# Kernel optimization log

Measured on AMD Instinct MI355X. Metric: run time of the kernel, lower is better.

## Reference

```python
import jax, jax.numpy as jnp
import numpy as np

B, A, FEAT = 16, 256, 64
HID = 256
TEMB = 32
NUM_T = 100
L = 4
E = 131072
N = B * A


def _remove_mean(x):
    # x: [B, A, 3]
    return x - jnp.mean(x, axis=1, keepdims=True)


def setup_inputs() -> dict:
    key = jax.random.key(0)
    ks = jax.random.split(key, 24)
    s = 0.02
    inp = {
        "h": jax.random.normal(ks[0], (B, A, FEAT), jnp.float32),
        "x0": jax.random.normal(ks[1], (B, A, 3), jnp.float32),
        "noise": jax.random.normal(ks[2], (B, A, 3), jnp.float32),
        "t": jax.random.randint(ks[3], (B,), 0, NUM_T, jnp.int32),
        "row": jax.random.randint(ks[4], (E,), 0, N, jnp.int32),
        "col": jax.random.randint(ks[5], (E,), 0, N, jnp.int32),
        # node embedding
        "W_emb": jax.random.normal(ks[6], (FEAT + TEMB, HID), jnp.float32) * s,
        "b_emb": jnp.zeros((HID,), jnp.float32),
        # per-layer EGNN params, stacked over L layers
        "eW1": jax.random.normal(ks[7], (L, 2 * HID + 1, HID), jnp.float32) * s,
        "eb1": jnp.zeros((L, HID), jnp.float32),
        "eW2": jax.random.normal(ks[8], (L, HID, HID), jnp.float32) * s,
        "eb2": jnp.zeros((L, HID), jnp.float32),
        "cW1": jax.random.normal(ks[9], (L, HID, HID), jnp.float32) * s,
        "cb1": jnp.zeros((L, HID), jnp.float32),
        "cW2": jax.random.normal(ks[10], (L, HID, 1), jnp.float32) * s,
        "nW1": jax.random.normal(ks[11], (L, 2 * HID, HID), jnp.float32) * s,
        "nb1": jnp.zeros((L, HID), jnp.float32),
        "nW2": jax.random.normal(ks[12], (L, HID, HID), jnp.float32) * s,
        "nb2": jnp.zeros((L, HID), jnp.float32),
    }
    return inp


def _time_embedding(t):
    half = TEMB // 2
    freq = jnp.exp(jnp.arange(half, dtype=jnp.float32) * (-np.log(10000.0) / (half - 1)))
    ang = t.astype(jnp.float32)[:, None] * freq[None, :]  # [B, half]
    return jnp.concatenate([jnp.sin(ang), jnp.cos(ang)], axis=-1)  # [B, TEMB]


def _egnn_layer(h, x, row, col, eW1, eb1, eW2, eb2, cW1, cb1, cW2, nW1, nb1, nW2, nb2):
    coord_diff = x[row] - x[col]                                  # [E, 3]
    radial = jnp.sum(coord_diff * coord_diff, axis=1, keepdims=True)  # [E, 1]
    edge_in = jnp.concatenate([h[row], h[col], radial], axis=1)   # [E, 2H+1]
    m = jax.nn.silu(edge_in @ eW1 + eb1)
    m_ij = jax.nn.silu(m @ eW2 + eb2)                             # [E, H]
    w = jax.nn.silu(m_ij @ cW1 + cb1) @ cW2                       # [E, 1]
    coord_update = coord_diff * w                                 # [E, 3]
    x_new = x + jax.ops.segment_sum(coord_update, row, num_segments=N)
    m_i = jax.ops.segment_sum(m_ij, row, num_segments=N)          # [N, H]
    node_in = jnp.concatenate([h, m_i], axis=1)
    h_new = h + (jax.nn.silu(node_in @ nW1 + nb1) @ nW2 + nb2)
    return h_new, x_new


def reference(h, x0, noise, W_emb, b_emb, eW1, eb1, eW2, eb2, cW1, cb1, cW2,
              nW1, nb1, nW2, nb2, t, row, col):
    # diffusion schedule
    betas = jnp.linspace(1e-4, 0.02, NUM_T, dtype=jnp.float32)
    alphas_cumprod = jnp.cumprod(1.0 - betas)
    # forward diffusion q(x_t | x_0)
    noise = _remove_mean(noise)
    ab = alphas_cumprod[t][:, None, None]                          # [B,1,1]
    xt = jnp.sqrt(ab) * x0 + jnp.sqrt(1.0 - ab) * noise
    xt = _remove_mean(xt)

    t_emb = _time_embedding(t)                                     # [B, TEMB]
    t_emb_flat = jnp.repeat(t_emb, A, axis=0)                      # [N, TEMB]
    h_flat = h.reshape(N, FEAT)
    xt_flat = xt.reshape(N, 3)
    h_in = jnp.concatenate([h_flat, t_emb_flat], axis=-1)

    hh = h_in @ W_emb + b_emb                                      # [N, H]
    xx = xt_flat
    for l in range(L):
        hh, xx = _egnn_layer(hh, xx, row, col,
                             eW1[l], eb1[l], eW2[l], eb2[l],
                             cW1[l], cb1[l], cW2[l],
                             nW1[l], nb1[l], nW2[l], nb2[l])

    noise_pred = (xx - xt_flat).reshape(B, A, 3)
    noise_pred = _remove_mean(noise_pred)
    loss = jnp.mean((noise_pred - noise) ** 2)
    return loss
```

## Files before the change

### kernel.cpp

```cpp
#include <hip/hip_runtime.h>

#define NB 16
#define NA 256
#define NNODES 4096
#define FEATD 64
#define HID 256
#define TEMBD 32
#define NUMT 100
#define NE 131072
#define NL 4
#define NCHUNK (NE / 16)

typedef __attribute__((ext_vector_type(8))) short short8;
typedef __attribute__((ext_vector_type(4))) float f32x4;
typedef __attribute__((ext_vector_type(2))) float f32x2;

__device__ __forceinline__ float silu_f(float v) {
    float s = __builtin_amdgcn_rcpf(1.f + __builtin_amdgcn_exp2f(-1.44269504f * v));
    return v * s;
}

__device__ __forceinline__ short f2bf(float f) {
    union { float f; unsigned u; } v; v.f = f;
    unsigned r = (v.u + 0x7fffu + ((v.u >> 16) & 1u)) >> 16;
    return (short)r;
}
__device__ __forceinline__ short f2bf_t(float f) {
    union { float f; unsigned u; } v; v.f = f;
    return (short)(v.u >> 16);
}
__device__ __forceinline__ float bf2f(short s) {
    union { float f; unsigned u; } v; v.u = ((unsigned)(unsigned short)s) << 16;
    return v.f;
}

__device__ __forceinline__ float block_sum(float v, float* red, int a) {
    red[a] = v; __syncthreads();
    for (int s = 128; s > 0; s >>= 1) {
        if (a < s) red[a] += red[a + s];
        __syncthreads();
    }
    float r = red[0]; __syncthreads();
    return r;
}

__global__ __launch_bounds__(256) void prep_kernel(
    const float* __restrict__ x0, const float* __restrict__ noise,
    const int* __restrict__ t,
    float* __restrict__ noise_c, float* __restrict__ xt, float* __restrict__ temb)
{
    __shared__ float red[256];
    __shared__ float sab_s[2];
    int b = blockIdx.x, a = threadIdx.x;
    int base = (b * NA + a) * 3;

    float nx = noise[base + 0], ny = noise[base + 1], nz = noise[base + 2];
    float mnx = block_sum(nx, red, a) * (1.f / NA);
    float mny = block_sum(ny, red, a) * (1.f / NA);
    float mnz = block_sum(nz, red, a) * (1.f / NA);
    nx -= mnx; ny -= mny; nz -= mnz;
    noise_c[base + 0] = nx; noise_c[base + 1] = ny; noise_c[base + 2] = nz;

    if (a == 0) {
        int tt = t[b];
        float p = 1.f;
        for (int i = 0; i < NUMT; i++) {
            float beta = 1e-4f + (0.02f - 1e-4f) * (float)i / (float)(NUMT - 1);
            if (i <= tt) p *= (1.f - beta);
        }
        sab_s[0] = sqrtf(p);
        sab_s[1] = sqrtf(1.f - p);
    }
    __syncthreads();
    float sab = sab_s[0], s1ab = sab_s[1];

    float xx = sab * x0[base + 0] + s1ab * nx;
    float xy = sab * x0[base + 1] + s1ab * ny;
    float xz = sab * x0[base + 2] + s1ab * nz;
    float mx = block_sum(xx, red, a) * (1.f / NA);
    float my = block_sum(xy, red, a) * (1.f / NA);
    float mz = block_sum(xz, red, a) * (1.f / NA);
    xt[base + 0] = xx - mx; xt[base + 1] = xy - my; xt[base + 2] = xz - mz;

    if (a < TEMBD / 2) {
        float fr = expf(-logf(10000.f) * (float)a / (float)(TEMBD / 2 - 1));
        float ang = (float)t[b] * fr;
        temb[b * TEMBD + a] = sinf(ang);
        temb[b * TEMBD + TEMBD / 2 + a] = cosf(ang);
    }
}

__global__ __launch_bounds__(256) void csr_hist(const int* __restrict__ row, int* __restrict__ deg)
{
    int i = blockIdx.x * 256 + threadIdx.x;
    if (i < NE) atomicAdd(&deg[row[i]], 1);
}

__global__ __launch_bounds__(256) void csr_scan(const int* __restrict__ deg, int* __restrict__ cursor)
{
    __shared__ int s[256];
    int t = threadIdx.x;
    int base = t * 16;
    int loc[16];
    int sum = 0;
    for (int i = 0; i < 16; i++) { loc[i] = sum; sum += deg[base + i]; }
    s[t] = sum; __syncthreads();
    for (int off = 1; off < 256; off <<= 1) {
        int v = (t >= off) ? s[t - off] : 0;
        __syncthreads();
        s[t] += v;
        __syncthreads();
    }
    int excl = (t == 0) ? 0 : s[t - 1];
    for (int i = 0; i < 16; i++) cursor[base + i] = excl + loc[i];
}

__global__ __launch_bounds__(256) void csr_scatter(
    const int* __restrict__ row, const int* __restrict__ col,
    int* __restrict__ cursor, int* __restrict__ prow, int* __restrict__ pcol)
{
    int i = blockIdx.x * 256 + threadIdx.x;
    if (i < NE) {
        int r = row[i];
        int p = atomicAdd(&cursor[r], 1);
        prow[p] = r;
        pcol[p] = col[i];
    }
}

#define WOFF_EMB 0
#define WOFF_L(l) (24576 + (l) * 458752)
#define WOFF_AB 0
#define WOFF_E2 131072
#define WOFF_C1 196608
#define WOFF_N1 262144
#define WOFF_N2 393216
#define W_TOTAL (24576 + 4 * 458752)

__global__ __launch_bounds__(256) void convert_weights(
    const float* __restrict__ W_emb, const float* __restrict__ eW1,
    const float* __restrict__ eW2, const float* __restrict__ cW1,
    const float* __restrict__ nW1, const float* __restrict__ nW2,
    short* __restrict__ wb)
{
    int idx = blockIdx.x * 256 + threadIdx.x;
    if (idx >= W_TOTAL) return;
    if (idx < 24576) {
        int k = idx >> 8, n = idx & 255;
        wb[WOFF_EMB + ((k >> 5) << 13) + (n << 5) + (k & 31)] = f2bf(W_emb[idx]);
        return;
    }
    int r = idx - 24576;
    int l = r / 458752;
    int o = r - l * 458752;
    if (o < 131072) {
        int k = o >> 9, n = o & 511;
        const float* src = eW1 + (size_t)l * 513 * 256 +
            (n < 256 ? (size_t)k * 256 + n : (size_t)(256 + k) * 256 + (n - 256));
        wb[WOFF_L(l) + WOFF_AB + ((k >> 5) * 16384) + (n << 5) + (k & 31)] = f2bf(*src);
        return;
    }
    const float* src; int dst; int o2;
    if (o < 196608)      { o2 = o - 131072; src = eW2 + (size_t)l * 65536 + o2;  dst = WOFF_L(l) + WOFF_E2; }
    else if (o < 262144) { o2 = o - 196608; src = cW1 + (size_t)l * 65536 + o2;  dst = WOFF_L(l) + WOFF_C1; }
    else if (o < 393216) { o2 = o - 262144; src = nW1 + (size_t)l * 131072 + o2; dst = WOFF_L(l) + WOFF_N1; }
    else                 { o2 = o - 393216; src = nW2 + (size_t)l * 65536 + o2;  dst = WOFF_L(l) + WOFF_N2; }
    int k = o2 >> 8, n = o2 & 255;
    wb[dst + ((k >> 5) << 13) + (n << 5) + (k & 31)] = f2bf(*src);
}

#define WF8_TOTAL (4 * 2 * 65536)
__global__ __launch_bounds__(256) void convert_weights_fp8(
    const float* __restrict__ eW2, const float* __restrict__ cW1,
    char* __restrict__ wf8)
{
    int idx = blockIdx.x * 256 + threadIdx.x;
    if (idx >= WF8_TOTAL) return;
    int l = idx >> 17;
    int o = idx & 131071;
    int mat = o >> 16;
    int o2 = o & 65535;
    int k = o2 >> 8, n = o2 & 255;
    const float* src = (mat == 0 ? eW2 : cW1) + (size_t)l * 65536 + (size_t)k * 256 + n;
    float v = (*src) * 16.f;
    int p = __builtin_amdgcn_cvt_pk_fp8_f32(v, v, 0, false);
    wf8[(size_t)l * 131072 + mat * 65536 + (k >> 5) * 8192 + n * 32 + (k & 31)] = (char)(p & 0xff);
}

__global__ __launch_bounds__(256) void build_hin(
    const float* __restrict__ h, const float* __restrict__ temb, short* __restrict__ hin)
{
    int idx = blockIdx.x * 256 + threadIdx.x;
    int n = idx / 96;
    int k = idx - n * 96;
    float v = (k < FEATD) ? h[n * FEATD + k] : temb[(n >> 8) * TEMBD + (k - FEATD)];
    hin[idx] = f2bf(v);
}

__global__ __launch_bounds__(512) void emb_p12_fused(
    const short* __restrict__ hin, const short* __restrict__ wtEmb,
    const float* __restrict__ b_emb, const short* __restrict__ wtAB,
    const float* __restrict__ eb1_0,
    short* __restrict__ hh, short* __restrict__ P12)
{
    __shared__ short h2s[16 * 264];
    int tid = threadIdx.x;
    int wv = tid >> 6, l = tid & 63;
    int lr = l & 15, q = l >> 4;
    int r0 = blockIdx.x * 16;

    f32x4 acc[2];
    #pragma unroll
    for (int i = 0; i < 2; i++) acc[i] = (f32x4){0.f, 0.f, 0.f, 0.f};
    #pragma unroll
    for (int kt = 0; kt < 3; kt++) {
        int kk = kt * 32 + q * 8;
        short8 fa = *(const short8*)&hin[(size_t)(r0 + lr) * 96 + kk];
        #pragma unroll
        for (int nt = 0; nt < 2; nt++) {
            short8 fb = *(const short8*)&wtEmb[kt * 8192 + (wv * 32 + nt * 16 + lr) * 32 + q * 8];
            acc[nt] = __builtin_amdgcn_mfma_f32_16x16x32_bf16(fa, fb, acc[nt], 0, 0, 0);
        }
    }
    #pragma unroll
    for (int nt = 0; nt < 2; nt++) {
        int col = wv * 32 + nt * 16 + lr;
        float bv = b_emb[col];
        #pragma unroll
        for (int rg = 0; rg < 4; rg++) {
            int rrow = q * 4 + rg;
            short b = f2bf(acc[nt][rg] + bv);
            hh[(size_t)(r0 + rrow) * 256 + col] = b;
            h2s[rrow * 264 + col] = b;
        }
    }
    __syncthreads();

    f32x4 acc3[4];
    #pragma unroll
    for (int i = 0; i < 4; i++) acc3[i] = (f32x4){0.f, 0.f, 0.f, 0.f};
    #pragma unroll 2
    for (int kt = 0; kt < 8; kt++) {
        short8 fa = *(const short8*)&h2s[lr * 264 + kt * 32 + q * 8];
        #pragma unroll
        for (int nt = 0; nt < 4; nt++) {
            short8 fb = *(const short8*)&wtAB[kt * 16384 + (wv * 64 + nt * 16 + lr) * 32 + q * 8];
            acc3[nt] = __builtin_amdgcn_mfma_f32_16x16x32_bf16(fa, fb, acc3[nt], 0, 0, 0);
        }
    }
    #pragma unroll
    for (int nt = 0; nt < 4; nt++) {
        int col = wv * 64 + nt * 16 + lr;
        float bv = (col < 256) ? eb1_0[col] : 0.f;
        #pragma unroll
        for (int rg = 0; rg < 4; rg++)
            P12[(size_t)(r0 + q * 4 + rg) * 512 + col] = f2bf(acc3[nt][rg] + bv);
    }
}

__global__ __launch_bounds__(512) void node_p12_fused(
    const short* __restrict__ hc, const float* __restrict__ m_i,
    const int* __restrict__ cursor,
    const int* __restrict__ tag0, const int* __restrict__ tag1,
    const float* __restrict__ msl0, const float* __restrict__ msl1,
    const float* __restrict__ xsl0, const float* __restrict__ xsl1,
    const float* __restrict__ x_agg, float* __restrict__ x_cur,
    const short* __restrict__ wtN1, const float* __restrict__ nb1,
    const short* __restrict__ wtN2, const float* __restrict__ nb2,
    const short* __restrict__ wtAB, const float* __restrict__ eb1n,
    short* __restrict__ hn, short* __restrict__ P12)
{
    __shared__ short m_is[16 * 264];
    __shared__ short t1s[16 * 264];
    __shared__ short h2s[16 * 264];
    int tid = threadIdx.x;
    int wv = tid >> 6, l = tid & 63;
    int lr = l & 15, q = l >> 4;
    int r0 = blockIdx.x * 16;

    {
        int rr = tid >> 5;
        int cc = (tid & 31) * 8;
        int r = r0 + rr;
        float v[8];
        const float* mrow = &m_i[(size_t)r * 256 + cc];
        #pragma unroll
        for (int i = 0; i < 8; i++) v[i] = mrow[i];
        int end = cursor[r];
        int start = (r == 0) ? 0 : cursor[r - 1];
        if (end > start) {
            int cs = start >> 4, ce = (end - 1) >> 4;
            for (int ch = cs; ch <= ce; ch++) {
                if (tag0[ch] == r) {
                    const float* s0 = &msl0[(size_t)ch * 256 + cc];
                    #pragma unroll
                    for (int i = 0; i < 8; i++) v[i] += s0[i];
                }
                if (tag1[ch] == r) {
                    const float* s1 = &msl1[(size_t)ch * 256 + cc];
                    #pragma unroll
                    for (int i = 0; i < 8; i++) v[i] += s1[i];
                }
            }
        }
        #pragma unroll
        for (int i = 0; i < 8; i++) m_is[rr * 264 + cc + i] = f2bf(v[i]);
        if (tid < 16) {
            int r2 = r0 + tid;
            float sx = x_agg[r2 * 3 + 0], sy = x_agg[r2 * 3 + 1], sz = x_agg[r2 * 3 + 2];
            int end2 = cursor[r2];
            int start2 = (r2 == 0) ? 0 : cursor[r2 - 1];
            if (end2 > start2) {
                int cs2 = start2 >> 4, ce2 = (end2 - 1) >> 4;
                for (int ch = cs2; ch <= ce2; ch++) {
                    if (tag0[ch] == r2) { sx += xsl0[ch * 3 + 0]; sy += xsl0[ch * 3 + 1]; sz += xsl0[ch * 3 + 2]; }
                    if (tag1[ch] == r2) { sx += xsl1[ch * 3 + 0]; sy += xsl1[ch * 3 + 1]; sz += xsl1[ch * 3 + 2]; }
                }
            }
            x_cur[r2 * 3 + 0] += sx;
            x_cur[r2 * 3 + 1] += sy;
            x_cur[r2 * 3 + 2] += sz;
        }
    }
    __syncthreads();

    f32x4 acc[2];
    #pragma unroll
    for (int i = 0; i < 2; i++) acc[i] = (f32x4){0.f, 0.f, 0.f, 0.f};
    #pragma unroll 2
    for (int kt = 0; kt < 16; kt++) {
        int kk = kt * 32 + q * 8;
        short8 fa;
        if (kk < 256) fa = *(const short8*)&hc[(size_t)(r0 + lr) * 256 + kk];
        else          fa = *(const short8*)&m_is[lr * 264 + kk - 256];
        #pragma unroll
        for (int nt = 0; nt < 2; nt++) {
            short8 fb = *(const short8*)&wtN1[kt * 8192 + (wv * 32 + nt * 16 + lr) * 32 + q * 8];
            acc[nt] = __builtin_amdgcn_mfma_f32_16x16x32_bf16(fa, fb, acc[nt], 0, 0, 0);
        }
    }
    #pragma unroll
    for (int nt = 0; nt < 2; nt++) {
        int col = wv * 32 + nt * 16 + lr;
        float bv = nb1[col];
        #pragma unroll
        for (int rg = 0; rg < 4; rg++)
            t1s[(q * 4 + rg) * 264 + col] = f2bf_t(silu_f(acc[nt][rg] + bv));
    }
    __syncthreads();

    f32x4 acc2[2];
    #pragma unroll
    for (int i = 0; i < 2; i++) acc2[i] = (f32x4){0.f, 0.f, 0.f, 0.f};
    #pragma unroll 2
    for (int kt = 0; kt < 8; kt++) {
        short8 fa = *(const short8*)&t1s[lr * 264 + kt * 32 + q * 8];
        #pragma unroll
        for (int nt = 0; nt < 2; nt++) {
            short8 fb = *(const short8*)&wtN2[kt * 8192 + (wv * 32 + nt * 16 + lr) * 32 + q * 8];
            acc2[nt] = __builtin_amdgcn_mfma_f32_16x16x32_bf16(fa, fb, acc2[nt], 0, 0, 0);
        }
    }
    #pragma unroll
    for (int nt = 0; nt < 2; nt++) {
        int col = wv * 32 + nt * 16 + lr;
        float bv = nb2[col];
        #pragma unroll
        for (int rg = 0; rg < 4; rg++) {
            int rrow = q * 4 + rg;
            float v = acc2[nt][rg] + bv + bf2f(hc[(size_t)(r0 + rrow) * 256 + col]);
            short b = f2bf(v);
            hn[(size_t)(r0 + rrow) * 256 + col] = b;
            h2s[rrow * 264 + col] = b;
        }
    }
    __syncthreads();

    f32x4 acc3[4];
    #pragma unroll
    for (int i = 0; i < 4; i++) acc3[i] = (f32x4){0.f, 0.f, 0.f, 0.f};
    #pragma unroll 2
    for (int kt = 0; kt < 8; kt++) {
        short8 fa = *(const short8*)&h2s[lr * 264 + kt * 32 + q * 8];
        #pragma unroll
        for (int nt = 0; nt < 4; nt++) {
            short8 fb = *(const short8*)&wtAB[kt * 16384 + (wv * 64 + nt * 16 + lr) * 32 + q * 8];
            acc3[nt] = __builtin_amdgcn_mfma_f32_16x16x32_bf16(fa, fb, acc3[nt], 0, 0, 0);
        }
    }
    #pragma unroll
    for (int nt = 0; nt < 4; nt++) {
        int col = wv * 64 + nt * 16 + lr;
        float bv = (col < 256) ? eb1n[col] : 0.f;
        #pragma unroll
        for (int rg = 0; rg < 4; rg++)
            P12[(size_t)(r0 + q * 4 + rg) * 512 + col] = f2bf(acc3[nt][rg] + bv);
    }
}

__global__ __launch_bounds__(256, 4) void egnn_edge_mfma(
    const short* __restrict__ P12, const float* __restrict__ x,
    const int* __restrict__ prow, const int* __restrict__ pcol,
    const float* __restrict__ w512,
    const char* __restrict__ wf8E2, const float* __restrict__ eb2,
    const char* __restrict__ wf8C1, const float* __restrict__ cb1,
    const float* __restrict__ cW2,
    float* __restrict__ m_i, float* __restrict__ x_agg,
    float* __restrict__ msl0, float* __restrict__ msl1,
    float* __restrict__ xsl0, float* __restrict__ xsl1,
    int* __restrict__ tag0, int* __restrict__ tag1, int do_mi)
{
    __shared__ __align__(16) char m_lds[64 * 272];
    __shared__ float cd_s[64][3];
    __shared__ int prow_s[64];
    __shared__ float wred[4][64];
    __shared__ float xtmp[64][3];

    int tid = threadIdx.x;
    int e0 = blockIdx.x * 64;
    int wv = tid >> 6, l = tid & 63;
    int lr = l & 15, q = l >> 4;

    {
        int e = tid >> 2, cq = tid & 3;
        int r = prow[e0 + e], c = pcol[e0 + e];
        float dx = x[r * 3 + 0] - x[c * 3 + 0];
        float dy = x[r * 3 + 1] - x[c * 3 + 1];
        float dz = x[r * 3 + 2] - x[c * 3 + 2];
        float rad = dx * dx + dy * dy + dz * dz;
        if (cq == 0) {
            prow_s[e] = r;
            cd_s[e][0] = dx; cd_s[e][1] = dy; cd_s[e][2] = dz;
        }
        const short* p1r = P12 + (size_t)r * 512;
        const short* p2r = P12 + (size_t)c * 512 + 256;
        #pragma unroll
        for (int j = 0; j < 8; j++) {
            int cb = (j >> 1) * 64 + (j & 1) * 32 + cq * 8;
            short8 a = *(const short8*)&p1r[cb];
            short8 b = *(const short8*)&p2r[cb];
            float4 w0 = *(const float4*)&w512[cb];
            float4 w1 = *(const float4*)&w512[cb + 4];
            float wv8[8] = {w0.x, w0.y, w0.z, w0.w, w1.x, w1.y, w1.z, w1.w};
            float s[8];
            #pragma unroll
            for (int k2 = 0; k2 < 8; k2++)
                s[k2] = silu_f(bf2f(a[k2]) + bf2f(b[k2]) + rad * wv8[k2]);
            int lo = __builtin_amdgcn_cvt_pk_fp8_f32(s[0], s[1], 0, false);
            lo = __builtin_amdgcn_cvt_pk_fp8_f32(s[2], s[3], lo, true);
            int hi = __builtin_amdgcn_cvt_pk_fp8_f32(s[4], s[5], 0, false);
            hi = __builtin_amdgcn_cvt_pk_fp8_f32(s[6], s[7], hi, true);
            int2 d = {lo, hi};
            *(int2*)&m_lds[e * 272 + cb] = d;
        }
    }
    __syncthreads();

    f32x4 acc[4][4];
    #pragma unroll
    for (int i = 0; i < 4; i++)
        #pragma unroll
        for (int j = 0; j < 4; j++) acc[i][j] = (f32x4){0.f, 0.f, 0.f, 0.f};
    #pragma unroll 2
    for (int kt = 0; kt < 8; kt++) {
        long fa[4], fb[4];
        #pragma unroll
        for (int mt = 0; mt < 4; mt++)
            fa[mt] = *(const long*)&m_lds[(mt * 16 + lr) * 272 + kt * 32 + q * 8];
        #pragma unroll
        for (int nt = 0; nt < 4; nt++)
            fb[nt] = *(const long*)&wf8E2[kt * 8192 + (wv * 64 + nt * 16 + lr) * 32 + q * 8];
        #pragma unroll
        for (int mt = 0; mt < 4; mt++)
            #pragma unroll
            for (int nt = 0; nt < 4; nt++)
                acc[mt][nt] = __builtin_amdgcn_mfma_f32_16x16x32_fp8_fp8(fa[mt], fb[nt], acc[mt][nt], 0, 0, 0);
    }
    __syncthreads();
    #pragma unroll
    for (int nt = 0; nt < 4; nt++) {
        int ccol = wv * 64 + nt * 16 + lr;
        float b2 = eb2[ccol];
        #pragma unroll
        for (int mt = 0; mt < 4; mt++)
            #pragma unroll
            for (int rg = 0; rg < 4; rg++) {
                int e = mt * 16 + q * 4 + rg;
                float v = silu_f(fmaf(acc[mt][nt][rg], 0.0625f, b2));
                int p = __builtin_amdgcn_cvt_pk_fp8_f32(v, v, 0, false);
                m_lds[e * 272 + ccol] = (char)(p & 0xff);
            }
    }
    __syncthreads();

    #pragma unroll
    for (int i = 0; i < 4; i++)
        #pragma unroll
        for (int j = 0; j < 4; j++) acc[i][j] = (f32x4){0.f, 0.f, 0.f, 0.f};
    #pragma unroll 2
    for (int kt = 0; kt < 8; kt++) {
        long fa[4], fb[4];
        #pragma unroll
        for (int mt = 0; mt < 4; mt++)
            fa[mt] = *(const long*)&m_lds[(mt * 16 + lr) * 272 + kt * 32 + q * 8];
        #pragma unroll
        for (int nt = 0; nt < 4; nt++)
            fb[nt] = *(const long*)&wf8C1[kt * 8192 + (wv * 64 + nt * 16 + lr) * 32 + q * 8];
        #pragma unroll
        for (int mt = 0; mt < 4; mt++)
            #pragma unroll
            for (int nt = 0; nt < 4; nt++)
                acc[mt][nt] = __builtin_amdgcn_mfma_f32_16x16x32_fp8_fp8(fa[mt], fb[nt], acc[mt][nt], 0, 0, 0);
    }

    if (do_mi) {
        int ebase = wv * 16;
        int c4 = l * 4;
        int chunk = blockIdx.x * 4 + wv;
        float a0 = 0.f, a1 = 0.f, a2 = 0.f, a3 = 0.f;
        int cur = prow_s[ebase];
        int nrun = 0;
        #pragma unroll
        for (int j = 0; j < 16; j++) {
            int e = ebase + j;
            int r = prow_s[e];
            if (r != cur) {
                float4 v = {a0, a1, a2, a3};
                if (nrun == 0) *(float4*)&msl0[(size_t)chunk * 256 + c4] = v;
                else           *(float4*)&m_i[(size_t)cur * 256 + c4] = v;
                nrun++; a0 = a1 = a2 = a3 = 0.f; cur = r;
            }
            int mv = *(const int*)&m_lds[e * 272 + c4];
            f32x2 lo = __builtin_amdgcn_cvt_pk_f32_fp8(mv, false);
            f32x2 hi = __builtin_amdgcn_cvt_pk_f32_fp8(mv, true);
            a0 += lo.x; a1 += lo.y; a2 += hi.x; a3 += hi.y;
        }
        float4 v = {a0, a1, a2, a3};
        if (nrun == 0) *(float4*)&msl0[(size_t)chunk * 256 + c4] = v;
        else           *(float4*)&msl1[(size_t)chunk * 256 + c4] = v;
        if (l == 0) {
            tag0[chunk] = prow_s[ebase];
            tag1[chunk] = nrun ? cur : -1;
        }
    }

    {
        float wp[4][4];
        #pragma unroll
        for (int i = 0; i < 4; i++)
            #pragma unroll
            for (int j = 0; j < 4; j++) wp[i][j] = 0.f;
        #pragma unroll
        for (int nt = 0; nt < 4; nt++) {
            int ccol = wv * 64 + nt * 16 + lr;
            float b1 = cb1[ccol];
            float c2 = cW2[ccol];
            #pragma unroll
            for (int mt = 0; mt < 4; mt++)
                #pragma unroll
                for (int rg = 0; rg < 4; rg++)
                    wp[mt][rg] += silu_f(fmaf(acc[mt][nt][rg], 0.0625f, b1)) * c2;
        }
        #pragma unroll
        for (int mt = 0; mt < 4; mt++)
            #pragma unroll
            for (int rg = 0; rg < 4; rg++) {
                float v = wp[mt][rg];
                v += __shfl_xor(v, 1, 64);
                v += __shfl_xor(v, 2, 64);
                v += __shfl_xor(v, 4, 64);
                v += __shfl_xor(v, 8, 64);
                if (lr == 0) wred[wv][mt * 16 + q * 4 + rg] = v;
            }
    }
    __syncthreads();
    if (tid < 64) {
        float w = wred[0][tid] + wred[1][tid] + wred[2][tid] + wred[3][tid];
        xtmp[tid][0] = cd_s[tid][0] * w;
        xtmp[tid][1] = cd_s[tid][1] * w;
        xtmp[tid][2] = cd_s[tid][2] * w;
    }
    __syncthreads();
    if (tid < 64) {
        int e = tid, j = e & 15, cw = e >> 4;
        int r = prow_s[e];
        bool leader = (j == 0) || (prow_s[e - 1] != r);
        if (leader) {
            int eend = (cw + 1) * 16;
            float sx = 0.f, sy = 0.f, sz = 0.f;
            int k = e;
            while (k < eend && prow_s[k] == r) {
                sx += xtmp[k][0]; sy += xtmp[k][1]; sz += xtmp[k][2]; k++;
            }
            int chunk = blockIdx.x * 4 + cw;
            if (j == 0)        { xsl0[chunk * 3 + 0] = sx; xsl0[chunk * 3 + 1] = sy; xsl0[chunk * 3 + 2] = sz; }
            else if (k == eend){ xsl1[chunk * 3 + 0] = sx; xsl1[chunk * 3 + 1] = sy; xsl1[chunk * 3 + 2] = sz; }
            else               { x_agg[r * 3 + 0] = sx; x_agg[r * 3 + 1] = sy; x_agg[r * 3 + 2] = sz; }
        }
    }
}

__global__ __launch_bounds__(256) void loss_part(
    const float* __restrict__ x_cur, const float* __restrict__ xt,
    const float* __restrict__ nc,
    const int* __restrict__ cursor,
    const int* __restrict__ tag0, const int* __restrict__ tag1,
    const float* __restrict__ xsl0, const float* __restrict__ xsl1,
    const float* __restrict__ x_agg,
    float* __restrict__ lpart)
{
    __shared__ float red[256];
    int b = blockIdx.x, a = threadIdx.x;
    int n = b * NA + a;
    int base = n * 3;

    float sx = x_agg[base + 0], sy = x_agg[base + 1], sz = x_agg[base + 2];
    int end = cursor[n];
    int start = (n == 0) ? 0 : cursor[n - 1];
    if (end > start) {
        int cs = start >> 4, ce = (end - 1) >> 4;
        for (int ch = cs; ch <= ce; ch++) {
            if (tag0[ch] == n) { sx += xsl0[ch * 3 + 0]; sy += xsl0[ch * 3 + 1]; sz += xsl0[ch * 3 + 2]; }
            if (tag1[ch] == n) { sx += xsl1[ch * 3 + 0]; sy += xsl1[ch * 3 + 1]; sz += xsl1[ch * 3 + 2]; }
        }
    }
    float px = x_cur[base + 0] + sx - xt[base + 0];
    float py = x_cur[base + 1] + sy - xt[base + 1];
    float pz = x_cur[base + 2] + sz - xt[base + 2];
    float mx = block_sum(px, red, a) * (1.f / NA);
    float my = block_sum(py, red, a) * (1.f / NA);
    float mz = block_sum(pz, red, a) * (1.f / NA);
    px -= mx; py -= my; pz -= mz;
    float dx = px - nc[base + 0], dy = py - nc[base + 1], dz = pz - nc[base + 2];
    float s = block_sum(dx * dx + dy * dy + dz * dz, red, a);
    if (a == 0) lpart[b] = s;
}

__global__ void loss_final(const float* __restrict__ lpart, float* __restrict__ out)
{
    if (threadIdx.x == 0) {
        float s = 0.f;
        for (int i = 0; i < NB; i++) s += lpart[i];
        out[0] = s / (float)(NNODES * 3);
    }
}

extern "C" void kernel_launch(void* const* d_in, const int* in_sizes, int n_in,
                              void* d_out, int out_size, void* d_ws, size_t ws_size,
                              hipStream_t stream)
{
    (void)in_sizes; (void)n_in; (void)out_size; (void)ws_size;
    const float* h     = (const float*)d_in[0];
    const float* x0    = (const float*)d_in[1];
    const float* noise = (const float*)d_in[2];
    const int*   t     = (const int*)d_in[3];
    const int*   row   = (const int*)d_in[4];
    const int*   col   = (const int*)d_in[5];
    const float* W_emb = (const float*)d_in[6];
    const float* b_emb = (const float*)d_in[7];
    const float* eW1   = (const float*)d_in[8];
    const float* eb1   = (const float*)d_in[9];
    const float* eW2   = (const float*)d_in[10];
    const float* eb2   = (const float*)d_in[11];
    const float* cW1   = (const float*)d_in[12];
    const float* cb1   = (const float*)d_in[13];
    const float* cW2   = (const float*)d_in[14];
    const float* nW1   = (const float*)d_in[15];
    const float* nb1   = (const float*)d_in[16];
    const float* nW2   = (const float*)d_in[17];
    const float* nb2   = (const float*)d_in[18];

    float* f = (float*)d_ws;
    size_t fo = 0;
    float* temb    = f + fo; fo += NB * TEMBD;
    float* noise_c = f + fo; fo += NNODES * 3;
    float* xt      = f + fo; fo += NNODES * 3;
    float* x_cur   = f + fo; fo += NNODES * 3;
    float* x_agg   = f + fo; fo += NNODES * 3;
    float* m_i     = f + fo; fo += (size_t)NNODES * HID;
    float* lpart   = f + fo; fo += NB;
    float* msl0    = f + fo; fo += (size_t)NCHUNK * 256;
    float* msl1    = f + fo; fo += (size_t)NCHUNK * 256;
    float* xsl0    = f + fo; fo += (size_t)NCHUNK * 3;
    float* xsl1    = f + fo; fo += (size_t)NCHUNK * 3;

    int* iw = (int*)(f + fo);
    size_t io = 0;
    int* deg    = iw + io; io += NNODES;
    int* cursor = iw + io; io += NNODES;
    int* prow   = iw + io; io += NE;
    int* pcol   = iw + io; io += NE;
    int* tag0   = iw + io; io += NCHUNK;
    int* tag1   = iw + io; io += NCHUNK;

    size_t sbase_bytes = ((((char*)(iw + io)) - (char*)d_ws) + 15) & ~(size_t)15;
    short* sb = (short*)((char*)d_ws + sbase_bytes);
    short* wb  = sb;
    size_t so = W_TOTAL;
    short* hin = sb + so; so += (size_t)NNODES * 96;
    short* hh  = sb + so; so += (size_t)NNODES * HID;
    short* hh2 = sb + so; so += (size_t)NNODES * HID;
    short* P12 = sb + so; so += (size_t)NNODES * 512;
    char* wf8 = (char*)(sb + so);

    prep_kernel<<<NB, 256, 0, stream>>>(x0, noise, t, noise_c, xt, temb);
    hipMemsetAsync(deg, 0, NNODES * sizeof(int), stream);
    csr_hist<<<NE / 256, 256, 0, stream>>>(row, deg);
    csr_scan<<<1, 256, 0, stream>>>(deg, cursor);
    csr_scatter<<<NE / 256, 256, 0, stream>>>(row, col, cursor, prow, pcol);
    convert_weights<<<(W_TOTAL + 255) / 256, 256, 0, stream>>>(W_emb, eW1, eW2, cW1, nW1, nW2, wb);
    convert_weights_fp8<<<WF8_TOTAL / 256, 256, 0, stream>>>(eW2, cW1, wf8);
    build_hin<<<(NNODES * 96) / 256, 256, 0, stream>>>(h, temb, hin);
    emb_p12_fused<<<NNODES / 16, 512, 0, stream>>>(
        hin, wb + WOFF_EMB, b_emb, wb + WOFF_L(0) + WOFF_AB, eb1, hh, P12);
    hipMemcpyAsync(x_cur, xt, (size_t)NNODES * 3 * sizeof(float), hipMemcpyDeviceToDevice, stream);

    short* hc = hh;
    short* hn = hh2;
    for (int l = 0; l < NL; l++) {
        const short* wl = wb + WOFF_L(l);
        const char* wf8l = wf8 + (size_t)l * 131072;
        int last = (l == NL - 1);
        size_t zcount = last ? (size_t)(NNODES * 3)
                             : (size_t)(NNODES * 3 + NNODES * HID);
        hipMemsetAsync(x_agg, 0, zcount * sizeof(float), stream);
        egnn_edge_mfma<<<NE / 64, 256, 0, stream>>>(
            P12, x_cur, prow, pcol,
            eW1 + (size_t)l * 513 * 256 + 512 * 256,
            wf8l, eb2 + (size_t)l * HID,
            wf8l + 65536, cb1 + (size_t)l * HID,
            cW2 + (size_t)l * HID,
            m_i, x_agg, msl0, msl1, xsl0, xsl1, tag0, tag1, last ? 0 : 1);
        if (!last) {
            node_p12_fused<<<NNODES / 16, 512, 0, stream>>>(
                hc, m_i, cursor, tag0, tag1, msl0, msl1,
                xsl0, xsl1, x_agg, x_cur,
                wl + WOFF_N1, nb1 + (size_t)l * HID,
                wl + WOFF_N2, nb2 + (size_t)l * HID,
                wb + WOFF_L(l + 1) + WOFF_AB, eb1 + (size_t)(l + 1) * HID,
                hn, P12);
            short* tmp = hc; hc = hn; hn = tmp;
        }
    }

    loss_part<<<NB, 256, 0, stream>>>(
        x_cur, xt, noise_c, cursor, tag0, tag1, xsl0, xsl1, x_agg, lpart);
    loss_final<<<1, 64, 0, stream>>>(lpart, (float*)d_out);
}
```

Before: 452.2 us.

## Drop per-layer memsets via interior-node flags, fuse build_hin and loss_final

Adds a csr_flag kernel that marks nodes whose edge ranges sit strictly inside a 16-edge chunk, so only those nodes read the atomically accumulated m_i/x_agg buffers. This lets the per-layer memsets of x_agg and m_i be removed. The deg memset moves into prep_kernel, build_hin is folded into emb_p12_fused with on-the-fly bf16 conversion, and loss_final is replaced by an atomicAdd into the output. The node and embedding kernels move to 1024-thread blocks with one 16-column tile per wave. Correctness depends on the edge kernel writing every non-flagged node's contribution only through the chunk slots, and on the atomic sum's ordering.

Result: faster. 440.5 us (-2.6%).

```diff
diff --git a/kernel.cpp b/kernel.cpp
--- a/kernel.cpp
+++ b/kernel.cpp
@@ -47,12 +47,16 @@
 __global__ __launch_bounds__(256) void prep_kernel(
     const float* __restrict__ x0, const float* __restrict__ noise,
     const int* __restrict__ t,
-    float* __restrict__ noise_c, float* __restrict__ xt, float* __restrict__ temb)
+    float* __restrict__ noise_c, float* __restrict__ xt, float* __restrict__ temb,
+    int* __restrict__ deg, float* __restrict__ out)
 {
     __shared__ float red[256];
     __shared__ float sab_s[2];
     int b = blockIdx.x, a = threadIdx.x;
     int base = (b * NA + a) * 3;
+
+    deg[b * 256 + a] = 0;
+    if (b == 0 && a == 0) out[0] = 0.f;
 
     float nx = noise[base + 0], ny = noise[base + 1], nz = noise[base + 2];
     float mnx = block_sum(nx, red, a) * (1.f / NA);
@@ -128,6 +132,25 @@
     }
 }
 
+__global__ __launch_bounds__(256) void csr_flag(
+    const int* __restrict__ cursor, int* __restrict__ flag)
+{
+    int r = blockIdx.x * 256 + threadIdx.x;
+    if (r >= NNODES) return;
+    int end = cursor[r];
+    int start = (r == 0) ? 0 : cursor[r - 1];
+    int fl = 0;
+    if (end > start) {
+        int cs = start >> 4, ce = (end - 1) >> 4;
+        for (int ch = cs; ch <= ce; ch++) {
+            int rs = start > ch * 16 ? start : ch * 16;
+            int re = end < ch * 16 + 16 ? end : ch * 16 + 16;
+            if (rs > ch * 16 && re < ch * 16 + 16) fl = 1;
+        }
+    }
+    flag[r] = fl;
+}
+
 #define WOFF_EMB 0
 #define WOFF_L(l) (24576 + (l) * 458752)
 #define WOFF_AB 0
@@ -187,18 +210,9 @@
     wf8[(size_t)l * 131072 + mat * 65536 + (k >> 5) * 8192 + n * 32 + (k & 31)] = (char)(p & 0xff);
 }
 
-__global__ __launch_bounds__(256) void build_hin(
-    const float* __restrict__ h, const float* __restrict__ temb, short* __restrict__ hin)
-{
-    int idx = blockIdx.x * 256 + threadIdx.x;
-    int n = idx / 96;
-    int k = idx - n * 96;
-    float v = (k < FEATD) ? h[n * FEATD + k] : temb[(n >> 8) * TEMBD + (k - FEATD)];
-    hin[idx] = f2bf(v);
-}
-
-__global__ __launch_bounds__(512) void emb_p12_fused(
-    const short* __restrict__ hin, const short* __restrict__ wtEmb,
+__global__ __launch_bounds__(1024) void emb_p12_fused(
+    const float* __restrict__ h, const float* __restrict__ temb,
+    const short* __restrict__ wtEmb,
     const float* __restrict__ b_emb, const short* __restrict__ wtAB,
     const float* __restrict__ eb1_0,
     short* __restrict__ hh, short* __restrict__ P12)
@@ -209,48 +223,47 @@
     int lr = l & 15, q = l >> 4;
     int r0 = blockIdx.x * 16;
 
-    f32x4 acc[2];
-    #pragma unroll
-    for (int i = 0; i < 2; i++) acc[i] = (f32x4){0.f, 0.f, 0.f, 0.f};
+    f32x4 acc = (f32x4){0.f, 0.f, 0.f, 0.f};
+    int col0 = wv * 16 + lr;
+    int n = r0 + lr;
     #pragma unroll
     for (int kt = 0; kt < 3; kt++) {
         int kk = kt * 32 + q * 8;
-        short8 fa = *(const short8*)&hin[(size_t)(r0 + lr) * 96 + kk];
+        const float* src = (kk < 64) ? &h[(size_t)n * 64 + kk]
+                                     : &temb[(n >> 8) * 32 + kk - 64];
+        short8 fa;
+        #pragma unroll
+        for (int k2 = 0; k2 < 8; k2++) fa[k2] = f2bf(src[k2]);
+        short8 fb = *(const short8*)&wtEmb[kt * 8192 + col0 * 32 + q * 8];
+        acc = __builtin_amdgcn_mfma_f32_16x16x32_bf16(fa, fb, acc, 0, 0, 0);
+    }
+    {
+        float bv = b_emb[col0];
+        #pragma unroll
+        for (int rg = 0; rg < 4; rg++) {
+            int rrow = q * 4 + rg;
+            short b = f2bf(acc[rg] + bv);
+            hh[(size_t)(r0 + rrow) * 256 + col0] = b;
+            h2s[rrow * 264 + col0] = b;
+        }
+    }
+    __syncthreads();
+
+    f32x4 acc3[2];
+    #pragma unroll
+    for (int i = 0; i < 2; i++) acc3[i] = (f32x4){0.f, 0.f, 0.f, 0.f};
+    #pragma unroll 2
+    for (int kt = 0; kt < 8; kt++) {
+        short8 fa = *(const short8*)&h2s[lr * 264 + kt * 32 + q * 8];
         #pragma unroll
         for (int nt = 0; nt < 2; nt++) {
-            short8 fb = *(const short8*)&wtEmb[kt * 8192 + (wv * 32 + nt * 16 + lr) * 32 + q * 8];
-            acc[nt] = __builtin_amdgcn_mfma_f32_16x16x32_bf16(fa, fb, acc[nt], 0, 0, 0);
+            short8 fb = *(const short8*)&wtAB[kt * 16384 + (wv * 32 + nt * 16 + lr) * 32 + q * 8];
+            acc3[nt] = __builtin_amdgcn_mfma_f32_16x16x32_bf16(fa, fb, acc3[nt], 0, 0, 0);
         }
     }
     #pragma unroll
     for (int nt = 0; nt < 2; nt++) {
         int col = wv * 32 + nt * 16 + lr;
-        float bv = b_emb[col];
-        #pragma unroll
-        for (int rg = 0; rg < 4; rg++) {
-            int rrow = q * 4 + rg;
-            short b = f2bf(acc[nt][rg] + bv);
-            hh[(size_t)(r0 + rrow) * 256 + col] = b;
-            h2s[rrow * 264 + col] = b;
-        }
-    }
-    __syncthreads();
-
-    f32x4 acc3[4];
-    #pragma unroll
-    for (int i = 0; i < 4; i++) acc3[i] = (f32x4){0.f, 0.f, 0.f, 0.f};
-    #pragma unroll 2
-    for (int kt = 0; kt < 8; kt++) {
-        short8 fa = *(const short8*)&h2s[lr * 264 + kt * 32 + q * 8];
-        #pragma unroll
-        for (int nt = 0; nt < 4; nt++) {
-            short8 fb = *(const short8*)&wtAB[kt * 16384 + (wv * 64 + nt * 16 + lr) * 32 + q * 8];
-            acc3[nt] = __builtin_amdgcn_mfma_f32_16x16x32_bf16(fa, fb, acc3[nt], 0, 0, 0);
-        }
-    }
-    #pragma unroll
-    for (int nt = 0; nt < 4; nt++) {
-        int col = wv * 64 + nt * 16 + lr;
         float bv = (col < 256) ? eb1_0[col] : 0.f;
         #pragma unroll
         for (int rg = 0; rg < 4; rg++)
@@ -258,9 +271,9 @@
     }
 }
 
-__global__ __launch_bounds__(512) void node_p12_fused(
+__global__ __launch_bounds__(1024) void node_p12_fused(
     const short* __restrict__ hc, const float* __restrict__ m_i,
-    const int* __restrict__ cursor,
+    const int* __restrict__ cursor, const int* __restrict__ flag,
     const int* __restrict__ tag0, const int* __restrict__ tag1,
     const float* __restrict__ msl0, const float* __restrict__ msl1,
     const float* __restrict__ xsl0, const float* __restrict__ xsl1,
@@ -279,35 +292,37 @@
     int r0 = blockIdx.x * 16;
 
     {
-        int rr = tid >> 5;
-        int cc = (tid & 31) * 8;
+        int rr = tid >> 6;
+        int cc = (tid & 63) * 4;
         int r = r0 + rr;
-        float v[8];
-        const float* mrow = &m_i[(size_t)r * 256 + cc];
-        #pragma unroll
-        for (int i = 0; i < 8; i++) v[i] = mrow[i];
+        float v[4] = {0.f, 0.f, 0.f, 0.f};
+        if (flag[r]) {
+            float4 mv = *(const float4*)&m_i[(size_t)r * 256 + cc];
+            v[0] = mv.x; v[1] = mv.y; v[2] = mv.z; v[3] = mv.w;
+        }
         int end = cursor[r];
         int start = (r == 0) ? 0 : cursor[r - 1];
         if (end > start) {
             int cs = start >> 4, ce = (end - 1) >> 4;
             for (int ch = cs; ch <= ce; ch++) {
                 if (tag0[ch] == r) {
-                    const float* s0 = &msl0[(size_t)ch * 256 + cc];
-                    #pragma unroll
-                    for (int i = 0; i < 8; i++) v[i] += s0[i];
+                    float4 s0 = *(const float4*)&msl0[(size_t)ch * 256 + cc];
+                    v[0] += s0.x; v[1] += s0.y; v[2] += s0.z; v[3] += s0.w;
                 }
                 if (tag1[ch] == r) {
-                    const float* s1 = &msl1[(size_t)ch * 256 + cc];
-                    #pragma unroll
-                    for (int i = 0; i < 8; i++) v[i] += s1[i];
+                    float4 s1 = *(const float4*)&msl1[(size_t)ch * 256 + cc];
+                    v[0] += s1.x; v[1] += s1.y; v[2] += s1.z; v[3] += s1.w;
                 }
             }
         }
         #pragma unroll
-        for (int i = 0; i < 8; i++) m_is[rr * 264 + cc + i] = f2bf(v[i]);
+        for (int i = 0; i < 4; i++) m_is[rr * 264 + cc + i] = f2bf(v[i]);
         if (tid < 16) {
             int r2 = r0 + tid;
-            float sx = x_agg[r2 * 3 + 0], sy = x_agg[r2 * 3 + 1], sz = x_agg[r2 * 3 + 2];
+            float sx = 0.f, sy = 0.f, sz = 0.f;
+            if (flag[r2]) {
+                sx = x_agg[r2 * 3 + 0]; sy = x_agg[r2 * 3 + 1]; sz = x_agg[r2 * 3 + 2];
+            }
             int end2 = cursor[r2];
             int start2 = (r2 == 0) ? 0 : cursor[r2 - 1];
             if (end2 > start2) {
@@ -324,73 +339,60 @@
     }
     __syncthreads();
 
-    f32x4 acc[2];
-    #pragma unroll
-    for (int i = 0; i < 2; i++) acc[i] = (f32x4){0.f, 0.f, 0.f, 0.f};
+    int col0 = wv * 16 + lr;
+    f32x4 acc = (f32x4){0.f, 0.f, 0.f, 0.f};
     #pragma unroll 2
     for (int kt = 0; kt < 16; kt++) {
         int kk = kt * 32 + q * 8;
         short8 fa;
         if (kk < 256) fa = *(const short8*)&hc[(size_t)(r0 + lr) * 256 + kk];
         else          fa = *(const short8*)&m_is[lr * 264 + kk - 256];
+        short8 fb = *(const short8*)&wtN1[kt * 8192 + col0 * 32 + q * 8];
+        acc = __builtin_amdgcn_mfma_f32_16x16x32_bf16(fa, fb, acc, 0, 0, 0);
+    }
+    {
+        float bv = nb1[col0];
+        #pragma unroll
+        for (int rg = 0; rg < 4; rg++)
+            t1s[(q * 4 + rg) * 264 + col0] = f2bf_t(silu_f(acc[rg] + bv));
+    }
+    __syncthreads();
+
+    f32x4 acc2 = (f32x4){0.f, 0.f, 0.f, 0.f};
+    #pragma unroll 2
+    for (int kt = 0; kt < 8; kt++) {
+        short8 fa = *(const short8*)&t1s[lr * 264 + kt * 32 + q * 8];
+        short8 fb = *(const short8*)&wtN2[kt * 8192 + col0 * 32 + q * 8];
+        acc2 = __builtin_amdgcn_mfma_f32_16x16x32_bf16(fa, fb, acc2, 0, 0, 0);
+    }
+    {
+        float bv = nb2[col0];
+        #pragma unroll
+        for (int rg = 0; rg < 4; rg++) {
+            int rrow = q * 4 + rg;
+            float v = acc2[rg] + bv + bf2f(hc[(size_t)(r0 + rrow) * 256 + col0]);
+            short b = f2bf(v);
+            hn[(size_t)(r0 + rrow) * 256 + col0] = b;
+            h2s[rrow * 264 + col0] = b;
+        }
+    }
+    __syncthreads();
+
+    f32x4 acc3[2];
+    #pragma unroll
+    for (int i = 0; i < 2; i++) acc3[i] = (f32x4){0.f, 0.f, 0.f, 0.f};
+    #pragma unroll 2
+    for (int kt = 0; kt < 8; kt++) {
+        short8 fa = *(const short8*)&h2s[lr * 264 + kt * 32 + q * 8];
         #pragma unroll
         for (int nt = 0; nt < 2; nt++) {
-            short8 fb = *(const short8*)&wtN1[kt * 8192 + (wv * 32 + nt * 16 + lr) * 32 + q * 8];
-            acc[nt] = __builtin_amdgcn_mfma_f32_16x16x32_bf16(fa, fb, acc[nt], 0, 0, 0);
+            short8 fb = *(const short8*)&wtAB[kt * 16384 + (wv * 32 + nt * 16 + lr) * 32 + q * 8];
+            acc3[nt] = __builtin_amdgcn_mfma_f32_16x16x32_bf16(fa, fb, acc3[nt], 0, 0, 0);
         }
     }
     #pragma unroll
     for (int nt = 0; nt < 2; nt++) {
         int col = wv * 32 + nt * 16 + lr;
-        float bv = nb1[col];
-        #pragma unroll
-        for (int rg = 0; rg < 4; rg++)
-            t1s[(q * 4 + rg) * 264 + col] = f2bf_t(silu_f(acc[nt][rg] + bv));
-    }
-    __syncthreads();
-
-    f32x4 acc2[2];
-    #pragma unroll
-    for (int i = 0; i < 2; i++) acc2[i] = (f32x4){0.f, 0.f, 0.f, 0.f};
-    #pragma unroll 2
-    for (int kt = 0; kt < 8; kt++) {
-        short8 fa = *(const short8*)&t1s[lr * 264 + kt * 32 + q * 8];
-        #pragma unroll
-        for (int nt = 0; nt < 2; nt++) {
-            short8 fb = *(const short8*)&wtN2[kt * 8192 + (wv * 32 + nt * 16 + lr) * 32 + q * 8];
-            acc2[nt] = __builtin_amdgcn_mfma_f32_16x16x32_bf16(fa, fb, acc2[nt], 0, 0, 0);
-        }
-    }
-    #pragma unroll
-    for (int nt = 0; nt < 2; nt++) {
-        int col = wv * 32 + nt * 16 + lr;
-        float bv = nb2[col];
-        #pragma unroll
-        for (int rg = 0; rg < 4; rg++) {
-            int rrow = q * 4 + rg;
-            float v = acc2[nt][rg] + bv + bf2f(hc[(size_t)(r0 + rrow) * 256 + col]);
-            short b = f2bf(v);
-            hn[(size_t)(r0 + rrow) * 256 + col] = b;
-            h2s[rrow * 264 + col] = b;
-        }
-    }
-    __syncthreads();
-
-    f32x4 acc3[4];
-    #pragma unroll
-    for (int i = 0; i < 4; i++) acc3[i] = (f32x4){0.f, 0.f, 0.f, 0.f};
-    #pragma unroll 2
-    for (int kt = 0; kt < 8; kt++) {
-        short8 fa = *(const short8*)&h2s[lr * 264 + kt * 32 + q * 8];
-        #pragma unroll
-        for (int nt = 0; nt < 4; nt++) {
-            short8 fb = *(const short8*)&wtAB[kt * 16384 + (wv * 64 + nt * 16 + lr) * 32 + q * 8];
-            acc3[nt] = __builtin_amdgcn_mfma_f32_16x16x32_bf16(fa, fb, acc3[nt], 0, 0, 0);
-        }
-    }
-    #pragma unroll
-    for (int nt = 0; nt < 4; nt++) {
-        int col = wv * 64 + nt * 16 + lr;
         float bv = (col < 256) ? eb1n[col] : 0.f;
         #pragma unroll
         for (int rg = 0; rg < 4; rg++)
@@ -603,18 +605,21 @@
 __global__ __launch_bounds__(256) void loss_part(
     const float* __restrict__ x_cur, const float* __restrict__ xt,
     const float* __restrict__ nc,
-    const int* __restrict__ cursor,
+    const int* __restrict__ cursor, const int* __restrict__ flag,
     const int* __restrict__ tag0, const int* __restrict__ tag1,
     const float* __restrict__ xsl0, const float* __restrict__ xsl1,
     const float* __restrict__ x_agg,
-    float* __restrict__ lpart)
+    float* __restrict__ out)
 {
     __shared__ float red[256];
     int b = blockIdx.x, a = threadIdx.x;
     int n = b * NA + a;
     int base = n * 3;
 
-    float sx = x_agg[base + 0], sy = x_agg[base + 1], sz = x_agg[base + 2];
+    float sx = 0.f, sy = 0.f, sz = 0.f;
+    if (flag[n]) {
+        sx = x_agg[base + 0]; sy = x_agg[base + 1]; sz = x_agg[base + 2];
+    }
     int end = cursor[n];
     int start = (n == 0) ? 0 : cursor[n - 1];
     if (end > start) {
@@ -633,16 +638,7 @@
     px -= mx; py -= my; pz -= mz;
     float dx = px - nc[base + 0], dy = py - nc[base + 1], dz = pz - nc[base + 2];
     float s = block_sum(dx * dx + dy * dy + dz * dz, red, a);
-    if (a == 0) lpart[b] = s;
-}
-
-__global__ void loss_final(const float* __restrict__ lpart, float* __restrict__ out)
-{
-    if (threadIdx.x == 0) {
-        float s = 0.f;
-        for (int i = 0; i < NB; i++) s += lpart[i];
-        out[0] = s / (float)(NNODES * 3);
-    }
+    if (a == 0) atomicAdd(out, s * (1.f / (float)(NNODES * 3)));
 }
 
 extern "C" void kernel_launch(void* const* d_in, const int* in_sizes, int n_in,
@@ -678,7 +674,6 @@
     float* x_cur   = f + fo; fo += NNODES * 3;
     float* x_agg   = f + fo; fo += NNODES * 3;
     float* m_i     = f + fo; fo += (size_t)NNODES * HID;
-    float* lpart   = f + fo; fo += NB;
     float* msl0    = f + fo; fo += (size_t)NCHUNK * 256;
     float* msl1    = f + fo; fo += (size_t)NCHUNK * 256;
     float* xsl0    = f + fo; fo += (size_t)NCHUNK * 3;
@@ -688,6 +683,7 @@
     size_t io = 0;
     int* deg    = iw + io; io += NNODES;
     int* cursor = iw + io; io += NNODES;
+    int* flag   = iw + io; io += NNODES;
     int* prow   = iw + io; io += NE;
     int* pcol   = iw + io; io += NE;
     int* tag0   = iw + io; io += NCHUNK;
@@ -697,22 +693,20 @@
     short* sb = (short*)((char*)d_ws + sbase_bytes);
     short* wb  = sb;
     size_t so = W_TOTAL;
-    short* hin = sb + so; so += (size_t)NNODES * 96;
     short* hh  = sb + so; so += (size_t)NNODES * HID;
     short* hh2 = sb + so; so += (size_t)NNODES * HID;
     short* P12 = sb + so; so += (size_t)NNODES * 512;
     char* wf8 = (char*)(sb + so);
 
-    prep_kernel<<<NB, 256, 0, stream>>>(x0, noise, t, noise_c, xt, temb);
-    hipMemsetAsync(deg, 0, NNODES * sizeof(int), stream);
+    prep_kernel<<<NB, 256, 0, stream>>>(x0, noise, t, noise_c, xt, temb, deg, (float*)d_out);
     csr_hist<<<NE / 256, 256, 0, stream>>>(row, deg);
     csr_scan<<<1, 256, 0, stream>>>(deg, cursor);
     csr_scatter<<<NE / 256, 256, 0, stream>>>(row, col, cursor, prow, pcol);
+    csr_flag<<<NNODES / 256, 256, 0, stream>>>(cursor, flag);
     convert_weights<<<(W_TOTAL + 255) / 256, 256, 0, stream>>>(W_emb, eW1, eW2, cW1, nW1, nW2, wb);
     convert_weights_fp8<<<WF8_TOTAL / 256, 256, 0, stream>>>(eW2, cW1, wf8);
-    build_hin<<<(NNODES * 96) / 256, 256, 0, stream>>>(h, temb, hin);
-    emb_p12_fused<<<NNODES / 16, 512, 0, stream>>>(
-        hin, wb + WOFF_EMB, b_emb, wb + WOFF_L(0) + WOFF_AB, eb1, hh, P12);
+    emb_p12_fused<<<NNODES / 16, 1024, 0, stream>>>(
+        h, temb, wb + WOFF_EMB, b_emb, wb + WOFF_L(0) + WOFF_AB, eb1, hh, P12);
     hipMemcpyAsync(x_cur, xt, (size_t)NNODES * 3 * sizeof(float), hipMemcpyDeviceToDevice, stream);
 
     short* hc = hh;
@@ -721,9 +715,6 @@
         const short* wl = wb + WOFF_L(l);
         const char* wf8l = wf8 + (size_t)l * 131072;
         int last = (l == NL - 1);
-        size_t zcount = last ? (size_t)(NNODES * 3)
-                             : (size_t)(NNODES * 3 + NNODES * HID);
-        hipMemsetAsync(x_agg, 0, zcount * sizeof(float), stream);
         egnn_edge_mfma<<<NE / 64, 256, 0, stream>>>(
             P12, x_cur, prow, pcol,
             eW1 + (size_t)l * 513 * 256 + 512 * 256,
@@ -732,8 +723,8 @@
             cW2 + (size_t)l * HID,
             m_i, x_agg, msl0, msl1, xsl0, xsl1, tag0, tag1, last ? 0 : 1);
         if (!last) {
-            node_p12_fused<<<NNODES / 16, 512, 0, stream>>>(
-                hc, m_i, cursor, tag0, tag1, msl0, msl1,
+            node_p12_fused<<<NNODES / 16, 1024, 0, stream>>>(
+                hc, m_i, cursor, flag, tag0, tag1, msl0, msl1,
                 xsl0, xsl1, x_agg, x_cur,
                 wl + WOFF_N1, nb1 + (size_t)l * HID,
                 wl + WOFF_N2, nb2 + (size_t)l * HID,
@@ -744,6 +735,5 @@
     }
 
     loss_part<<<NB, 256, 0, stream>>>(
-        x_cur, xt, noise_c, cursor, tag0, tag1, xsl0, xsl1, x_agg, lpart);
-    loss_final<<<1, 64, 0, stream>>>(lpart, (float*)d_out);
-}
+        x_cur, xt, noise_c, cursor, flag, tag0, tag1, xsl0, xsl1, x_agg, (float*)d_out);
+}
```
